# Optimization experiments

Measured on AMD Instinct MI355X. Metric: run time of the kernel, lower is better.

The kernel has to match this reference:

```python
import jax, jax.numpy as jnp
import numpy as np

N_NODES = 50000
N_EDGES = 800000
F_IN = 128
HIDDEN = 128
N_CLASSES = 40


def setup_inputs() -> dict:
    key = jax.random.key(0)
    ks = jax.random.split(key, 8)
    x = jax.random.normal(ks[0], (N_NODES, F_IN), dtype=jnp.float32)
    edge_index = jax.random.randint(ks[1], (2, N_EDGES), 0, N_NODES, dtype=jnp.int32)
    s_in = 1.0 / np.sqrt(F_IN)
    s_h = 1.0 / np.sqrt(HIDDEN)
    W1_l = jax.random.normal(ks[2], (F_IN, HIDDEN), jnp.float32) * s_in
    W1_r = jax.random.normal(ks[3], (F_IN, HIDDEN), jnp.float32) * s_in
    b1 = jnp.zeros((HIDDEN,), jnp.float32)
    W2_l = jax.random.normal(ks[4], (HIDDEN, N_CLASSES), jnp.float32) * s_h
    W2_r = jax.random.normal(ks[5], (HIDDEN, N_CLASSES), jnp.float32) * s_h
    b2 = jnp.zeros((N_CLASSES,), jnp.float32)
    return {"x": x, "edge_index": edge_index, "W1_l": W1_l, "W1_r": W1_r,
            "b1": b1, "W2_l": W2_l, "W2_r": W2_r, "b2": b2}


def _sage_conv(x, src, dst, W_l, W_r, b):
    # mean-aggregate neighbor features at dst, then linear transform + root weight
    msg = x[src]                                                  # [E, d] gather
    agg = jax.ops.segment_sum(msg, dst, num_segments=N_NODES)     # [N, d] scatter-add
    deg = jax.ops.segment_sum(jnp.ones((src.shape[0],), x.dtype), dst,
                              num_segments=N_NODES)
    agg = agg / jnp.maximum(deg, 1.0)[:, None]                    # mean aggregation
    return agg @ W_l + x @ W_r + b


def reference(x, edge_index, W1_l, W1_r, b1, W2_l, W2_r, b2):
    src, dst = edge_index[0], edge_index[1]
    h = jax.nn.relu(_sage_conv(x, src, dst, W1_l, W1_r, b1))
    # F.dropout(p=0.5, training=self.training) -> identity in eval mode
    out = jax.nn.relu(_sage_conv(h, src, dst, W2_l, W2_r, b2))
    return jax.nn.log_softmax(out, axis=-1)
```

## Files before the change

kernel.cpp:

```cpp
#include <hip/hip_runtime.h>

#define N_NODES 50000
#define N_EDGES 800000
#define F_IN 128
#define HIDDEN 128
#define N_CLASSES 40

#define NBUCKET 196
#define BUCKET_CAP 8192
#define BINA_CHUNK 4096
#define BINA_NBLK 196
#define PREP_ITEMS (N_NODES * 32 + 128 * 256 + 80 * 128)
#define PREP_NBLK (PREP_ITEMS / 256)

#define OFF_RS     0
#define OFF_BCNT   50004
#define OFF_INVDEG 100004
#define OFF_SRCS   150004
#define OFF_AB     950004
#define OFF_PB     950004
#define OFF_Q      2950004
#define OFF_BINS   7350004
#define OFF_HB     7350004
#define OFF_WT1    10550004
#define OFF_WT2    10566388

typedef short bf16x8 __attribute__((ext_vector_type(8)));
typedef float f32x4 __attribute__((ext_vector_type(4)));
typedef unsigned short u16x8 __attribute__((ext_vector_type(8)));

static __device__ __forceinline__ unsigned short f2bf(float f) {
  unsigned int u = __builtin_bit_cast(unsigned int, f);
  u = (u + 0x7fffu + ((u >> 16) & 1u)) >> 16;
  return (unsigned short)u;
}
static __device__ __forceinline__ float bf2f(unsigned short s) {
  unsigned int u = ((unsigned int)s) << 16;
  return __builtin_bit_cast(float, u);
}

__global__ __launch_bounds__(256) void k_binA_prep(
    const int* __restrict__ src, const int* __restrict__ dst,
    int* __restrict__ bcnt, int* __restrict__ bins,
    const float* __restrict__ x, const float* __restrict__ W1l,
    const float* __restrict__ W1r, const float* __restrict__ W2l,
    const float* __restrict__ W2r, unsigned short* __restrict__ Ab,
    unsigned short* __restrict__ Wt1, unsigned short* __restrict__ Wt2) {
  if (blockIdx.x >= BINA_NBLK) {
    int idx = (blockIdx.x - BINA_NBLK) * 256 + threadIdx.x;
    if (idx < N_NODES * 32) {
      int row = idx >> 5, c4 = (idx & 31) << 2;
      const float4 v = *(const float4*)(x + (size_t)row * F_IN + c4);
      ushort4 o;
      o.x = f2bf(v.x); o.y = f2bf(v.y); o.z = f2bf(v.z); o.w = f2bf(v.w);
      *(ushort4*)(Ab + (size_t)row * 256 + 128 + c4) = o;
      return;
    }
    idx -= N_NODES * 32;
    if (idx < 128 * 256) {
      int n = idx >> 8, k = idx & 255;
      float v = (k < 128) ? W1l[(size_t)k * 128 + n]
                          : W1r[(size_t)(k - 128) * 128 + n];
      Wt1[(size_t)n * 256 + k] = f2bf(v);
    } else if (idx < 128 * 256 + 80 * 128) {
      int j = idx - 128 * 256;
      int n = j >> 7, k = j & 127;
      float v = (n < 40) ? W2l[(size_t)k * 40 + n]
                         : W2r[(size_t)k * 40 + (n - 40)];
      Wt2[(size_t)n * 128 + k] = f2bf(v);
    }
    return;
  }
  __shared__ int cnt[NBUCKET];
  __shared__ int excl[NBUCKET];
  __shared__ int cursor[NBUCKET];
  __shared__ int bbase[NBUCKET];
  __shared__ int sc[256];
  __shared__ int stage[BINA_CHUNK];
  __shared__ unsigned char bkt[BINA_CHUNK];
  int t = threadIdx.x;
  int e0 = blockIdx.x * BINA_CHUNK;
  int ne = N_EDGES - e0;
  if (ne > BINA_CHUNK) ne = BINA_CHUNK;
  if (t < NBUCKET) cnt[t] = 0;
  __syncthreads();
  for (int i = t; i < ne; i += 256) atomicAdd(&cnt[dst[e0 + i] >> 8], 1);
  __syncthreads();
  int v = (t < NBUCKET) ? cnt[t] : 0;
  sc[t] = v;
  __syncthreads();
  for (int off = 1; off < 256; off <<= 1) {
    int add = (t >= off) ? sc[t - off] : 0;
    __syncthreads();
    sc[t] += add;
    __syncthreads();
  }
  if (t < NBUCKET) {
    int ex = sc[t] - v;
    excl[t] = ex;
    cursor[t] = ex;
    bbase[t] = atomicAdd(&bcnt[t], v);
  }
  __syncthreads();
  for (int i = t; i < ne; i += 256) {
    int d = dst[e0 + i];
    int s = src[e0 + i];
    int b = d >> 8;
    int pos = atomicAdd(&cursor[b], 1);
    stage[pos] = ((d & 255) << 16) | s;
    bkt[pos] = (unsigned char)b;
  }
  __syncthreads();
  for (int i = t; i < ne; i += 256) {
    int b = bkt[i];
    bins[(size_t)b * BUCKET_CAP + bbase[b] + (i - excl[b])] = stage[i];
  }
}

__global__ __launch_bounds__(256) void k_binB(
    const int* __restrict__ bcnt, const int* __restrict__ bins,
    int* __restrict__ rs, int* __restrict__ srcs,
    float* __restrict__ invdeg) {
  __shared__ int sc[256];
  __shared__ int hist[256];
  __shared__ int cursor[256];
  int b = blockIdx.x;
  int t = threadIdx.x;
  sc[t] = (t < NBUCKET && t < b) ? bcnt[t] : 0;
  __syncthreads();
  for (int off = 128; off; off >>= 1) {
    if (t < off) sc[t] += sc[t + off];
    __syncthreads();
  }
  int base = sc[0];
  int cnt = bcnt[b];
  const int* bb = bins + (size_t)b * BUCKET_CAP;
  hist[t] = 0;
  __syncthreads();
  for (int i = t; i < cnt; i += 256) atomicAdd(&hist[bb[i] >> 16], 1);
  __syncthreads();
  int c = hist[t];
  sc[t] = c;
  __syncthreads();
  for (int off = 1; off < 256; off <<= 1) {
    int add = (t >= off) ? sc[t - off] : 0;
    __syncthreads();
    sc[t] += add;
    __syncthreads();
  }
  int lexcl = sc[t] - c;
  int node = b * 256 + t;
  if (node < N_NODES) {
    rs[node] = base + lexcl;
    invdeg[node] = 1.0f / (float)(c > 1 ? c : 1);
  }
  if (b == 0 && t == 0) rs[N_NODES] = N_EDGES;
  cursor[t] = lexcl;
  __syncthreads();
  for (int i = t; i < cnt; i += 256) {
    int v = bb[i];
    int pos = atomicAdd(&cursor[v >> 16], 1);
    srcs[base + pos] = v & 0xFFFF;
  }
}

__global__ __launch_bounds__(256) void k_gather1(
    const int* __restrict__ rs, const int* __restrict__ srcs,
    const float* __restrict__ invdeg, unsigned short* __restrict__ Ab) {
  int node = blockIdx.x * 4 + (threadIdx.x >> 6);
  int lane = threadIdx.x & 63;
  int slot = lane >> 3, li = lane & 7;
  if (node >= N_NODES) return;
  int beg = rs[node], end = rs[node + 1];
  float acc[16];
#pragma unroll
  for (int j = 0; j < 16; j++) acc[j] = 0.f;
  for (int i = beg + slot; i < end; i += 8) {
    int s = srcs[i];
    const unsigned short* rp = Ab + (size_t)s * 256 + 128 + li * 8;
    u16x8 v0 = *(const u16x8*)rp;
    u16x8 v1 = *(const u16x8*)(rp + 64);
#pragma unroll
    for (int j = 0; j < 8; j++) {
      acc[j] += bf2f(v0[j]);
      acc[8 + j] += bf2f(v1[j]);
    }
  }
#pragma unroll
  for (int off = 8; off <= 32; off <<= 1)
#pragma unroll
    for (int j = 0; j < 16; j++) acc[j] += __shfl_xor(acc[j], off, 64);
  if (slot == 0) {
    float inv = invdeg[node];
    u16x8 o0, o1;
#pragma unroll
    for (int j = 0; j < 8; j++) {
      o0[j] = f2bf(acc[j] * inv);
      o1[j] = f2bf(acc[8 + j] * inv);
    }
    *(u16x8*)(Ab + (size_t)node * 256 + li * 8) = o0;
    *(u16x8*)(Ab + (size_t)node * 256 + 64 + li * 8) = o1;
  }
}

__global__ __launch_bounds__(256) void k_l1(
    const unsigned short* __restrict__ Ab, const unsigned short* __restrict__ Wt1,
    const float* __restrict__ b1, unsigned short* __restrict__ hb) {
  int w = threadIdx.x >> 6, lane = threadIdx.x & 63;
  int r = lane & 15, quad = lane >> 4;
  int row0 = blockIdx.x * 64 + w * 16;
  int arow = row0 + r;
  if (arow >= N_NODES) arow = N_NODES - 1;
  const unsigned short* Ap = Ab + (size_t)arow * 256 + quad * 8;
  const unsigned short* Bp = Wt1 + (size_t)r * 256 + quad * 8;
  f32x4 acc[8];
#pragma unroll
  for (int n = 0; n < 8; n++) acc[n] = (f32x4){0.f, 0.f, 0.f, 0.f};
#pragma unroll
  for (int k0 = 0; k0 < 256; k0 += 32) {
    bf16x8 af = *(const bf16x8*)(Ap + k0);
#pragma unroll
    for (int n = 0; n < 8; n++) {
      bf16x8 bv = *(const bf16x8*)(Bp + (size_t)n * 16 * 256 + k0);
      acc[n] = __builtin_amdgcn_mfma_f32_16x16x32_bf16(af, bv, acc[n], 0, 0, 0);
    }
  }
  int crow0 = row0 + quad * 4;
#pragma unroll
  for (int n = 0; n < 8; n++) {
    int col = n * 16 + r;
    float bias = b1[col];
#pragma unroll
    for (int reg = 0; reg < 4; reg++) {
      int row = crow0 + reg;
      if (row < N_NODES)
        hb[(size_t)row * HIDDEN + col] = f2bf(fmaxf(acc[n][reg] + bias, 0.f));
    }
  }
}

__global__ __launch_bounds__(256) void k_pq(
    const unsigned short* __restrict__ hb, const unsigned short* __restrict__ Wt2,
    const float* __restrict__ b2, unsigned short* __restrict__ pb,
    float* __restrict__ q) {
  int w = threadIdx.x >> 6, lane = threadIdx.x & 63;
  int r = lane & 15, quad = lane >> 4;
  int row0 = blockIdx.x * 64 + w * 16;
  int arow = row0 + r;
  if (arow >= N_NODES) arow = N_NODES - 1;
  const unsigned short* Ap = hb + (size_t)arow * HIDDEN + quad * 8;
  const unsigned short* Bp = Wt2 + (size_t)r * 128 + quad * 8;
  f32x4 acc[5];
#pragma unroll
  for (int n = 0; n < 5; n++) acc[n] = (f32x4){0.f, 0.f, 0.f, 0.f};
#pragma unroll
  for (int k0 = 0; k0 < 128; k0 += 32) {
    bf16x8 af = *(const bf16x8*)(Ap + k0);
#pragma unroll
    for (int n = 0; n < 5; n++) {
      bf16x8 bv = *(const bf16x8*)(Bp + (size_t)n * 16 * 128 + k0);
      acc[n] = __builtin_amdgcn_mfma_f32_16x16x32_bf16(af, bv, acc[n], 0, 0, 0);
    }
  }
  int crow0 = row0 + quad * 4;
#pragma unroll
  for (int n = 0; n < 5; n++) {
    int col = n * 16 + r;
#pragma unroll
    for (int reg = 0; reg < 4; reg++) {
      int row = crow0 + reg;
      if (row < N_NODES) {
        float v = acc[n][reg];
        if (col < N_CLASSES)
          pb[(size_t)row * 40 + col] = f2bf(v);
        else
          q[(size_t)row * N_CLASSES + (col - N_CLASSES)] = v + b2[col - N_CLASSES];
      }
    }
  }
}

__global__ __launch_bounds__(256) void k_final(
    const unsigned short* __restrict__ pb, const float* __restrict__ q,
    const int* __restrict__ rs, const int* __restrict__ srcs,
    const float* __restrict__ invdeg, float* __restrict__ out) {
  int node = blockIdx.x * 4 + (threadIdx.x >> 6);
  int lane = threadIdx.x & 63;
  int slot = lane >> 3, li = lane & 7;
  if (node >= N_NODES) return;
  bool valid = li < 5;
  int beg = rs[node], end = rs[node + 1];
  float acc[8];
#pragma unroll
  for (int j = 0; j < 8; j++) acc[j] = 0.f;
  for (int i = beg + slot; i < end; i += 8) {
    int s = srcs[i];
    if (valid) {
      u16x8 v = *(const u16x8*)(pb + (size_t)s * 40 + li * 8);
#pragma unroll
      for (int j = 0; j < 8; j++) acc[j] += bf2f(v[j]);
    }
  }
#pragma unroll
  for (int off = 8; off <= 32; off <<= 1)
#pragma unroll
    for (int j = 0; j < 8; j++) acc[j] += __shfl_xor(acc[j], off, 64);
  float inv = invdeg[node];
  float v[8];
  float m = -1e30f;
  if (valid) {
    const float* qr = q + (size_t)node * N_CLASSES + li * 8;
    float4 q0 = *(const float4*)qr;
    float4 q1 = *(const float4*)(qr + 4);
    v[0] = fmaxf(acc[0] * inv + q0.x, 0.f);
    v[1] = fmaxf(acc[1] * inv + q0.y, 0.f);
    v[2] = fmaxf(acc[2] * inv + q0.z, 0.f);
    v[3] = fmaxf(acc[3] * inv + q0.w, 0.f);
    v[4] = fmaxf(acc[4] * inv + q1.x, 0.f);
    v[5] = fmaxf(acc[5] * inv + q1.y, 0.f);
    v[6] = fmaxf(acc[6] * inv + q1.z, 0.f);
    v[7] = fmaxf(acc[7] * inv + q1.w, 0.f);
#pragma unroll
    for (int j = 0; j < 8; j++) m = fmaxf(m, v[j]);
  }
#pragma unroll
  for (int off = 1; off <= 4; off <<= 1) m = fmaxf(m, __shfl_xor(m, off, 8));
  float ssum = 0.f;
  if (valid) {
#pragma unroll
    for (int j = 0; j < 8; j++) ssum += __expf(v[j] - m);
  }
#pragma unroll
  for (int off = 1; off <= 4; off <<= 1) ssum += __shfl_xor(ssum, off, 8);
  float lse = __logf(ssum) + m;
  if (slot == 0 && valid) {
    float* orow = out + (size_t)node * N_CLASSES + li * 8;
    *(float4*)orow = make_float4(v[0] - lse, v[1] - lse, v[2] - lse, v[3] - lse);
    *(float4*)(orow + 4) =
        make_float4(v[4] - lse, v[5] - lse, v[6] - lse, v[7] - lse);
  }
}

extern "C" void kernel_launch(void* const* d_in, const int* in_sizes, int n_in,
                              void* d_out, int out_size, void* d_ws,
                              size_t ws_size, hipStream_t stream) {
  const float* x   = (const float*)d_in[0];
  const int*   ei  = (const int*)d_in[1];
  const int*   src = ei;
  const int*   dst = ei + N_EDGES;
  const float* W1l = (const float*)d_in[2];
  const float* W1r = (const float*)d_in[3];
  const float* b1  = (const float*)d_in[4];
  const float* W2l = (const float*)d_in[5];
  const float* W2r = (const float*)d_in[6];
  const float* b2  = (const float*)d_in[7];
  float* out = (float*)d_out;

  float* wsf = (float*)d_ws;
  int*   rs     = (int*)wsf + OFF_RS;
  int*   bcnt   = (int*)wsf + OFF_BCNT;
  float* invdeg = wsf + OFF_INVDEG;
  int*   srcs   = (int*)wsf + OFF_SRCS;
  unsigned short* Ab  = (unsigned short*)(wsf + OFF_AB);
  unsigned short* pb  = (unsigned short*)(wsf + OFF_PB);
  unsigned short* hb  = (unsigned short*)(wsf + OFF_HB);
  unsigned short* Wt1 = (unsigned short*)(wsf + OFF_WT1);
  unsigned short* Wt2 = (unsigned short*)(wsf + OFF_WT2);
  int*   bins   = (int*)wsf + OFF_BINS;
  float* q = wsf + OFF_Q;

  hipMemsetAsync(bcnt, 0, NBUCKET * sizeof(int), stream);

  k_binA_prep<<<BINA_NBLK + PREP_NBLK, 256, 0, stream>>>(
      src, dst, bcnt, bins, x, W1l, W1r, W2l, W2r, Ab, Wt1, Wt2);
  k_binB<<<NBUCKET, 256, 0, stream>>>(bcnt, bins, rs, srcs, invdeg);
  k_gather1<<<(N_NODES + 3) / 4, 256, 0, stream>>>(rs, srcs, invdeg, Ab);
  k_l1<<<(N_NODES + 63) / 64, 256, 0, stream>>>(Ab, Wt1, b1, hb);
  k_pq<<<(N_NODES + 63) / 64, 256, 0, stream>>>(hb, Wt2, b2, pb, q);
  k_final<<<(N_NODES + 3) / 4, 256, 0, stream>>>(pb, q, rs, srcs, invdeg, out);
}
```

Before: 240.6 us.

## Fuse layer-1 and layer-2 linear kernels through LDS and halve bucket size

Merges the layer-1 GEMM and the layer-2 projection into one kernel that keeps the hidden activations in shared memory instead of writing and re-reading an hb buffer in global memory, which also removes one launch. Separately, edge binning switches from 256-node buckets to 128-node buckets, doubling the bucket count and halving the chunk size so the binning and CSR-build kernels get more, smaller blocks. The prefix scan now handles two buckets per thread. Costs include extra LDS use and a block barrier in the fused MLP, plus more global atomics on the bucket counters.

```diff
diff --git a/kernel.cpp b/kernel.cpp
--- a/kernel.cpp
+++ b/kernel.cpp
@@ -6,10 +6,10 @@
 #define HIDDEN 128
 #define N_CLASSES 40
 
-#define NBUCKET 196
-#define BUCKET_CAP 8192
-#define BINA_CHUNK 4096
-#define BINA_NBLK 196
+#define NBUCKET 391
+#define BUCKET_CAP 4096
+#define BINA_CHUNK 2048
+#define BINA_NBLK 391
 #define PREP_ITEMS (N_NODES * 32 + 128 * 256 + 80 * 128)
 #define PREP_NBLK (PREP_ITEMS / 256)
 
@@ -21,7 +21,6 @@
 #define OFF_PB     950004
 #define OFF_Q      2950004
 #define OFF_BINS   7350004
-#define OFF_HB     7350004
 #define OFF_WT1    10550004
 #define OFF_WT2    10566388
 
@@ -77,17 +76,19 @@
   __shared__ int bbase[NBUCKET];
   __shared__ int sc[256];
   __shared__ int stage[BINA_CHUNK];
-  __shared__ unsigned char bkt[BINA_CHUNK];
+  __shared__ unsigned short bkt[BINA_CHUNK];
   int t = threadIdx.x;
   int e0 = blockIdx.x * BINA_CHUNK;
   int ne = N_EDGES - e0;
   if (ne > BINA_CHUNK) ne = BINA_CHUNK;
-  if (t < NBUCKET) cnt[t] = 0;
-  __syncthreads();
-  for (int i = t; i < ne; i += 256) atomicAdd(&cnt[dst[e0 + i] >> 8], 1);
-  __syncthreads();
-  int v = (t < NBUCKET) ? cnt[t] : 0;
-  sc[t] = v;
+  for (int i = t; i < NBUCKET; i += 256) cnt[i] = 0;
+  __syncthreads();
+  for (int i = t; i < ne; i += 256) atomicAdd(&cnt[dst[e0 + i] >> 7], 1);
+  __syncthreads();
+  int a = (2 * t < NBUCKET) ? cnt[2 * t] : 0;
+  int b2_ = (2 * t + 1 < NBUCKET) ? cnt[2 * t + 1] : 0;
+  int s = a + b2_;
+  sc[t] = s;
   __syncthreads();
   for (int off = 1; off < 256; off <<= 1) {
     int add = (t >= off) ? sc[t - off] : 0;
@@ -95,20 +96,22 @@
     sc[t] += add;
     __syncthreads();
   }
-  if (t < NBUCKET) {
-    int ex = sc[t] - v;
-    excl[t] = ex;
-    cursor[t] = ex;
-    bbase[t] = atomicAdd(&bcnt[t], v);
-  }
+  int pbase = sc[t] - s;
+  if (2 * t < NBUCKET) { excl[2 * t] = pbase; cursor[2 * t] = pbase; }
+  if (2 * t + 1 < NBUCKET) {
+    excl[2 * t + 1] = pbase + a;
+    cursor[2 * t + 1] = pbase + a;
+  }
+  for (int i = t; i < NBUCKET; i += 256)
+    bbase[i] = atomicAdd(&bcnt[i], cnt[i]);
   __syncthreads();
   for (int i = t; i < ne; i += 256) {
     int d = dst[e0 + i];
-    int s = src[e0 + i];
-    int b = d >> 8;
+    int sv = src[e0 + i];
+    int b = d >> 7;
     int pos = atomicAdd(&cursor[b], 1);
-    stage[pos] = ((d & 255) << 16) | s;
-    bkt[pos] = (unsigned char)b;
+    stage[pos] = ((d & 127) << 16) | sv;
+    bkt[pos] = (unsigned short)b;
   }
   __syncthreads();
   for (int i = t; i < ne; i += 256) {
@@ -122,11 +125,14 @@
     int* __restrict__ rs, int* __restrict__ srcs,
     float* __restrict__ invdeg) {
   __shared__ int sc[256];
-  __shared__ int hist[256];
-  __shared__ int cursor[256];
+  __shared__ int hist[128];
+  __shared__ int cursor[128];
   int b = blockIdx.x;
   int t = threadIdx.x;
-  sc[t] = (t < NBUCKET && t < b) ? bcnt[t] : 0;
+  int v = 0;
+  if (t < b) v += bcnt[t];
+  if (t + 256 < b) v += bcnt[t + 256];
+  sc[t] = v;
   __syncthreads();
   for (int off = 128; off; off >>= 1) {
     if (t < off) sc[t] += sc[t + off];
@@ -135,32 +141,32 @@
   int base = sc[0];
   int cnt = bcnt[b];
   const int* bb = bins + (size_t)b * BUCKET_CAP;
-  hist[t] = 0;
+  if (t < 128) hist[t] = 0;
   __syncthreads();
   for (int i = t; i < cnt; i += 256) atomicAdd(&hist[bb[i] >> 16], 1);
   __syncthreads();
-  int c = hist[t];
+  int c = (t < 128) ? hist[t] : 0;
   sc[t] = c;
   __syncthreads();
-  for (int off = 1; off < 256; off <<= 1) {
+  for (int off = 1; off < 128; off <<= 1) {
     int add = (t >= off) ? sc[t - off] : 0;
     __syncthreads();
     sc[t] += add;
     __syncthreads();
   }
   int lexcl = sc[t] - c;
-  int node = b * 256 + t;
-  if (node < N_NODES) {
+  int node = b * 128 + t;
+  if (t < 128 && node < N_NODES) {
     rs[node] = base + lexcl;
     invdeg[node] = 1.0f / (float)(c > 1 ? c : 1);
   }
   if (b == 0 && t == 0) rs[N_NODES] = N_EDGES;
-  cursor[t] = lexcl;
+  if (t < 128) cursor[t] = lexcl;
   __syncthreads();
   for (int i = t; i < cnt; i += 256) {
-    int v = bb[i];
-    int pos = atomicAdd(&cursor[v >> 16], 1);
-    srcs[base + pos] = v & 0xFFFF;
+    int v2 = bb[i];
+    int pos = atomicAdd(&cursor[v2 >> 16], 1);
+    srcs[base + pos] = v2 & 0xFFFF;
   }
 }
 
@@ -203,9 +209,12 @@
   }
 }
 
-__global__ __launch_bounds__(256) void k_l1(
+__global__ __launch_bounds__(256) void k_mlp(
     const unsigned short* __restrict__ Ab, const unsigned short* __restrict__ Wt1,
-    const float* __restrict__ b1, unsigned short* __restrict__ hb) {
+    const unsigned short* __restrict__ Wt2, const float* __restrict__ b1,
+    const float* __restrict__ b2, unsigned short* __restrict__ pb,
+    float* __restrict__ q) {
+  __shared__ unsigned short hs[64 * 132];
   int w = threadIdx.x >> 6, lane = threadIdx.x & 63;
   int r = lane & 15, quad = lane >> 4;
   int row0 = blockIdx.x * 64 + w * 16;
@@ -225,41 +234,33 @@
       acc[n] = __builtin_amdgcn_mfma_f32_16x16x32_bf16(af, bv, acc[n], 0, 0, 0);
     }
   }
-  int crow0 = row0 + quad * 4;
+  int lrow0 = w * 16 + quad * 4;
 #pragma unroll
   for (int n = 0; n < 8; n++) {
     int col = n * 16 + r;
     float bias = b1[col];
 #pragma unroll
-    for (int reg = 0; reg < 4; reg++) {
-      int row = crow0 + reg;
-      if (row < N_NODES)
-        hb[(size_t)row * HIDDEN + col] = f2bf(fmaxf(acc[n][reg] + bias, 0.f));
-    }
-  }
-}
-
-__global__ __launch_bounds__(256) void k_pq(
-    const unsigned short* __restrict__ hb, const unsigned short* __restrict__ Wt2,
-    const float* __restrict__ b2, unsigned short* __restrict__ pb,
-    float* __restrict__ q) {
-  int w = threadIdx.x >> 6, lane = threadIdx.x & 63;
-  int r = lane & 15, quad = lane >> 4;
-  int row0 = blockIdx.x * 64 + w * 16;
-  int arow = row0 + r;
-  if (arow >= N_NODES) arow = N_NODES - 1;
-  const unsigned short* Ap = hb + (size_t)arow * HIDDEN + quad * 8;
-  const unsigned short* Bp = Wt2 + (size_t)r * 128 + quad * 8;
-  f32x4 acc[5];
-#pragma unroll
-  for (int n = 0; n < 5; n++) acc[n] = (f32x4){0.f, 0.f, 0.f, 0.f};
+    for (int reg = 0; reg < 4; reg++)
+      hs[(lrow0 + reg) * 132 + col] = f2bf(fmaxf(acc[n][reg] + bias, 0.f));
+  }
+  __syncthreads();
+  int lr = w * 16 + r;
+  const unsigned short* Bp2 = Wt2 + (size_t)r * 128 + quad * 8;
+  f32x4 acc2[5];
+#pragma unroll
+  for (int n = 0; n < 5; n++) acc2[n] = (f32x4){0.f, 0.f, 0.f, 0.f};
 #pragma unroll
   for (int k0 = 0; k0 < 128; k0 += 32) {
-    bf16x8 af = *(const bf16x8*)(Ap + k0);
+    const unsigned short* hp = &hs[lr * 132 + k0 + quad * 8];
+    ushort4 h0 = *(const ushort4*)hp;
+    ushort4 h1 = *(const ushort4*)(hp + 4);
+    bf16x8 af;
+    af[0] = (short)h0.x; af[1] = (short)h0.y; af[2] = (short)h0.z; af[3] = (short)h0.w;
+    af[4] = (short)h1.x; af[5] = (short)h1.y; af[6] = (short)h1.z; af[7] = (short)h1.w;
 #pragma unroll
     for (int n = 0; n < 5; n++) {
-      bf16x8 bv = *(const bf16x8*)(Bp + (size_t)n * 16 * 128 + k0);
-      acc[n] = __builtin_amdgcn_mfma_f32_16x16x32_bf16(af, bv, acc[n], 0, 0, 0);
+      bf16x8 bv = *(const bf16x8*)(Bp2 + (size_t)n * 16 * 128 + k0);
+      acc2[n] = __builtin_amdgcn_mfma_f32_16x16x32_bf16(af, bv, acc2[n], 0, 0, 0);
     }
   }
   int crow0 = row0 + quad * 4;
@@ -270,7 +271,7 @@
     for (int reg = 0; reg < 4; reg++) {
       int row = crow0 + reg;
       if (row < N_NODES) {
-        float v = acc[n][reg];
+        float v = acc2[n][reg];
         if (col < N_CLASSES)
           pb[(size_t)row * 40 + col] = f2bf(v);
         else
@@ -363,7 +364,6 @@
   int*   srcs   = (int*)wsf + OFF_SRCS;
   unsigned short* Ab  = (unsigned short*)(wsf + OFF_AB);
   unsigned short* pb  = (unsigned short*)(wsf + OFF_PB);
-  unsigned short* hb  = (unsigned short*)(wsf + OFF_HB);
   unsigned short* Wt1 = (unsigned short*)(wsf + OFF_WT1);
   unsigned short* Wt2 = (unsigned short*)(wsf + OFF_WT2);
   int*   bins   = (int*)wsf + OFF_BINS;
@@ -375,7 +375,6 @@
       src, dst, bcnt, bins, x, W1l, W1r, W2l, W2r, Ab, Wt1, Wt2);
   k_binB<<<NBUCKET, 256, 0, stream>>>(bcnt, bins, rs, srcs, invdeg);
   k_gather1<<<(N_NODES + 3) / 4, 256, 0, stream>>>(rs, srcs, invdeg, Ab);
-  k_l1<<<(N_NODES + 63) / 64, 256, 0, stream>>>(Ab, Wt1, b1, hb);
-  k_pq<<<(N_NODES + 63) / 64, 256, 0, stream>>>(hb, Wt2, b2, pb, q);
+  k_mlp<<<(N_NODES + 63) / 64, 256, 0, stream>>>(Ab, Wt1, Wt2, b1, b2, pb, q);
   k_final<<<(N_NODES + 3) / 4, 256, 0, stream>>>(pb, q, rs, srcs, invdeg, out);
 }
```

Result: faster. 233.4 us (-3.0%).
